# Performance work log

Measured on AMD Instinct MI355X. Metric: run time of the kernel, lower is better.

## Reference

```python
import jax, jax.numpy as jnp
import numpy as np

PADDING = 2  # matches init_kwargs; kernel_size = 2*PADDING + 1 -> no circular wrap in roll trick


def setup_inputs() -> dict:
    key = jax.random.key(0)
    k1, k2, k3 = jax.random.split(key, 3)
    x = jax.random.normal(k1, (16, 512, 4096), dtype=jnp.float32)
    weight = jax.random.normal(k2, (512, 512, 5), dtype=jnp.float32)
    bias = jax.random.normal(k3, (512,), dtype=jnp.float32)
    return {"x": x, "weight": weight, "bias": bias}


def reference(x, weight, bias):
    # Original torch module: pad(p,p) -> cat of roll(n-p) copies -> slice -> matmul.
    # Index algebra: out[b,o,t] = sum_{c,n} w[o,c,n] * xpad[b,c, t + 2p - n],
    # which (with kernel_size == 2p+1, so no circular wraparound) is a true
    # convolution, i.e. cross-correlation with the kernel flipped along taps.
    w_flipped = jnp.flip(weight, axis=-1)  # [O, I, K]
    y = jax.lax.conv_general_dilated(
        x, w_flipped,
        window_strides=(1,),
        padding=[(PADDING, PADDING)],
        dimension_numbers=("NCH", "OIH", "NCH"),
    )  # [B, O, T]
    return y + bias[None, :, None]
```

## Files before the change

### kernel.cpp

```cpp
#include <hip/hip_runtime.h>
#include <hip/hip_bf16.h>

typedef __attribute__((ext_vector_type(8))) short short8;
typedef __attribute__((ext_vector_type(4))) float f32x4;

#define B_   16
#define O_   512
#define C_   512
#define T_   4096
#define TP   (T_ + 32)
#define KT   5
#define BM   128
#define BN   512
#define BK   32
#define NCHUNK (C_/BK)
#define AFR  40
#define BGR  33

__device__ __forceinline__ void gload_lds16(const void* g, void* l) {
    __builtin_amdgcn_global_load_lds(
        (const __attribute__((address_space(1))) unsigned int*)g,
        (__attribute__((address_space(3))) unsigned int*)l, 16, 0, 0);
}

__global__ void wrepack_kernel(const float* __restrict__ w, unsigned short* __restrict__ wb) {
    int e = blockIdx.x * 256 + threadIdx.x;
    if (e >= KT * O_ * C_) return;
    int n   = e / (O_ * C_);
    int rem = e % (O_ * C_);
    int o   = rem / C_;
    int c   = rem % C_;
    float v = w[((size_t)o * C_ + c) * KT + n];
    __hip_bfloat16 h = __float2bfloat16(v);
    wb[e] = *reinterpret_cast<unsigned short*>(&h);
}

__global__ void padzero_kernel(unsigned short* __restrict__ xt) {
    int i = blockIdx.x * 256 + threadIdx.x;
    if (i >= B_ * 32 * C_) return;
    int b = i / (32 * C_);
    int r = (i / C_) % 32;
    int c = i % C_;
    int tp = (r < 16) ? r : (T_ + r);
    xt[((size_t)b * TP + tp) * C_ + c] = 0;
}

__global__ void xtrans_kernel(const float* __restrict__ x, unsigned short* __restrict__ xt) {
    __shared__ float tile[64][65];
    int b  = blockIdx.z;
    int c0 = blockIdx.y * 64;
    int t0 = blockIdx.x * 64;
    const float* xb = x + ((size_t)b * C_ + c0) * T_ + t0;
#pragma unroll
    for (int p = 0; p < 4; ++p) {
        int idx = p * 256 + threadIdx.x;
        int cl = idx >> 4;
        int tj = (idx & 15) << 2;
        float4 v = *reinterpret_cast<const float4*>(xb + (size_t)cl * T_ + tj);
        tile[cl][tj + 0] = v.x;
        tile[cl][tj + 1] = v.y;
        tile[cl][tj + 2] = v.z;
        tile[cl][tj + 3] = v.w;
    }
    __syncthreads();
    unsigned short* xtb = xt + ((size_t)b * TP + 16 + t0) * C_ + c0;
#pragma unroll
    for (int p = 0; p < 2; ++p) {
        int g  = p * 256 + threadIdx.x;
        int tl = g >> 3;
        int cj = (g & 7) << 3;
        unsigned short tmp[8];
#pragma unroll
        for (int i = 0; i < 8; ++i) {
            __hip_bfloat16 h = __float2bfloat16(tile[cj + i][tl]);
            tmp[i] = *reinterpret_cast<unsigned short*>(&h);
        }
        *reinterpret_cast<short8*>(xtb + (size_t)tl * C_ + cj) =
            *reinterpret_cast<const short8*>(tmp);
    }
}

__global__ __launch_bounds__(512, 2) void conv_gemm_kernel(
        const unsigned short* __restrict__ wb,
        const unsigned short* __restrict__ xt,
        const float* __restrict__ bias,
        float* __restrict__ out) {
    __shared__ unsigned short a_lds[2][AFR * 512];
    __shared__ unsigned short b_lds[2][BGR * 512];

    int bid = blockIdx.x;
    int swz = (bid & 7) * 64 + (bid >> 3);
    int o0  = (swz & 3) * BM;
    int t0  = ((swz >> 2) & 7) * BN;
    int b   = swz >> 5;

    int tid  = threadIdx.x;
    int lane = tid & 63;
    int wid  = tid >> 6;
    int lr   = lane & 15;
    int lg   = lane >> 4;

    int bo[KT][4];
#pragma unroll
    for (int n = 0; n < KT; ++n)
#pragma unroll
        for (int ni = 0; ni < 4; ++ni) {
            int row = wid * 64 + ni * 16 + lr + 4 - n;
            bo[n][ni] = row * 32 + ((lg ^ ((row >> 1) & 3)) << 3);
        }

    f32x4 acc[8][4];
#pragma unroll
    for (int mi = 0; mi < 8; ++mi)
#pragma unroll
        for (int ni = 0; ni < 4; ++ni)
            acc[mi][ni] = (f32x4)0.0f;

    const unsigned short* ag = wb + (size_t)(o0 + lr) * C_ + lg * 8;
    int c8 = (lane & 3) ^ ((lane >> 3) & 3);
    const unsigned short* bg = xt + ((size_t)b * TP + (t0 + 14 + (lane >> 2))) * C_ + c8 * 8;

#pragma unroll
    for (int f = wid; f < AFR; f += 8)
        gload_lds16(ag + (size_t)((f >> 3) * O_ + (f & 7) * 16) * C_, &a_lds[0][f * 512]);
#pragma unroll
    for (int j = wid; j < BGR; j += 8)
        gload_lds16(bg + (size_t)(j * 16) * C_, &b_lds[0][j * 512]);
    asm volatile("s_waitcnt vmcnt(0)" ::: "memory");
    __builtin_amdgcn_s_barrier();

    for (int chunk = 0; chunk < NCHUNK; ++chunk) {
        int cur = chunk & 1;
        int c1  = (chunk + 1) * BK;
        bool pf = (chunk + 1 < NCHUNK);

#pragma unroll
        for (int n = 0; n < KT; ++n) {
            short8 af[8], bf[4];
#pragma unroll
            for (int mi = 0; mi < 8; ++mi)
                af[mi] = *reinterpret_cast<const short8*>(
                    &a_lds[cur][(n * 8 + mi) * 512 + lane * 8]);
#pragma unroll
            for (int ni = 0; ni < 4; ++ni)
                bf[ni] = *reinterpret_cast<const short8*>(&b_lds[cur][bo[n][ni]]);

            if (pf) {
                int f = n * 8 + wid;
                gload_lds16(ag + (size_t)((f >> 3) * O_ + (f & 7) * 16) * C_ + c1,
                            &a_lds[cur ^ 1][f * 512]);
                int j = n * 8 + wid;
                if (j < BGR)
                    gload_lds16(bg + (size_t)(j * 16) * C_ + c1, &b_lds[cur ^ 1][j * 512]);
            }

            __builtin_amdgcn_s_barrier();
            asm volatile("s_waitcnt lgkmcnt(0)" ::: "memory");
            __builtin_amdgcn_sched_barrier(0);

            __builtin_amdgcn_s_setprio(1);
#pragma unroll
            for (int mi = 0; mi < 8; ++mi)
#pragma unroll
                for (int ni = 0; ni < 4; ++ni)
                    acc[mi][ni] = __builtin_amdgcn_mfma_f32_16x16x32_bf16(
                        af[mi], bf[ni], acc[mi][ni], 0, 0, 0);
            __builtin_amdgcn_s_setprio(0);
        }

        asm volatile("s_waitcnt vmcnt(0)" ::: "memory");
        __builtin_amdgcn_s_barrier();
    }

#pragma unroll
    for (int mi = 0; mi < 8; ++mi) {
#pragma unroll
        for (int ni = 0; ni < 4; ++ni) {
            int orow = o0 + mi * 16 + lg * 4;
            int tcol = t0 + wid * 64 + ni * 16 + lr;
#pragma unroll
            for (int r = 0; r < 4; ++r) {
                out[((size_t)b * O_ + orow + r) * T_ + tcol] =
                    acc[mi][ni][r] + bias[orow + r];
            }
        }
    }
}

extern "C" void kernel_launch(void* const* d_in, const int* in_sizes, int n_in,
                              void* d_out, int out_size, void* d_ws, size_t ws_size,
                              hipStream_t stream) {
    const float* x    = (const float*)d_in[0];
    const float* w    = (const float*)d_in[1];
    const float* bias = (const float*)d_in[2];
    float* out        = (float*)d_out;

    unsigned short* wb  = (unsigned short*)d_ws;
    unsigned short* xtp = wb + (size_t)KT * O_ * C_;

    padzero_kernel<<<(B_ * 32 * C_ + 255) / 256, 256, 0, stream>>>(xtp);
    wrepack_kernel<<<(KT * O_ * C_ + 255) / 256, 256, 0, stream>>>(w, wb);
    xtrans_kernel<<<dim3(T_ / 64, C_ / 64, B_), 256, 0, stream>>>(x, xtp);
    conv_gemm_kernel<<<512, 512, 0, stream>>>(wb, xtp, bias, out);
}
```

Baseline: 193.6 us.

## Issue all chunk prefetches up front and double-buffer tap fragments in registers

All global-to-LDS prefetches for the next chunk are now issued at the start of each chunk instead of being spread across the five taps. The per-tap barrier and lgkmcnt wait are removed. LDS fragment loads are ping-ponged between two register sets so the next tap's reads overlap the current tap's MFMAs. This cuts four barriers per chunk and adds software pipelining, at the cost of more VGPR pressure from holding two fragment sets alongside the 128-float accumulator under launch_bounds(512,2).

After: 199.6 us. +3.1%, slower.

```diff
diff --git a/kernel.cpp b/kernel.cpp
--- a/kernel.cpp
+++ b/kernel.cpp
@@ -80,6 +80,29 @@
     }
 }
 
+#define LOADTAP(n, AF, BF)                                                         \
+    do {                                                                           \
+        _Pragma("unroll")                                                          \
+        for (int mi = 0; mi < 8; ++mi)                                             \
+            AF[mi] = *reinterpret_cast<const short8*>(                             \
+                &al[((n) * 8 + mi) * 512 + lane * 8]);                             \
+        _Pragma("unroll")                                                          \
+        for (int ni = 0; ni < 4; ++ni)                                             \
+            BF[ni] = *reinterpret_cast<const short8*>(&bl[bo[(n)][ni]]);           \
+    } while (0)
+
+#define MFMATAP(AF, BF)                                                            \
+    do {                                                                           \
+        __builtin_amdgcn_s_setprio(1);                                             \
+        _Pragma("unroll")                                                          \
+        for (int mi = 0; mi < 8; ++mi)                                             \
+            _Pragma("unroll")                                                      \
+            for (int ni = 0; ni < 4; ++ni)                                         \
+                acc[mi][ni] = __builtin_amdgcn_mfma_f32_16x16x32_bf16(             \
+                    AF[mi], BF[ni], acc[mi][ni], 0, 0, 0);                         \
+        __builtin_amdgcn_s_setprio(0);                                             \
+    } while (0)
+
 __global__ __launch_bounds__(512, 2) void conv_gemm_kernel(
         const unsigned short* __restrict__ wb,
         const unsigned short* __restrict__ xt,
@@ -121,55 +144,50 @@
     const unsigned short* bg = xt + ((size_t)b * TP + (t0 + 14 + (lane >> 2))) * C_ + c8 * 8;
 
 #pragma unroll
-    for (int f = wid; f < AFR; f += 8)
-        gload_lds16(ag + (size_t)((f >> 3) * O_ + (f & 7) * 16) * C_, &a_lds[0][f * 512]);
-#pragma unroll
-    for (int j = wid; j < BGR; j += 8)
-        gload_lds16(bg + (size_t)(j * 16) * C_, &b_lds[0][j * 512]);
+    for (int k = 0; k < 5; ++k)
+        gload_lds16(ag + (size_t)(k * O_ + wid * 16) * C_, &a_lds[0][(wid + 8 * k) * 512]);
+#pragma unroll
+    for (int k = 0; k < 5; ++k) {
+        int j = wid + 8 * k;
+        if (j < BGR)
+            gload_lds16(bg + (size_t)(j * 16) * C_, &b_lds[0][j * 512]);
+    }
     asm volatile("s_waitcnt vmcnt(0)" ::: "memory");
     __builtin_amdgcn_s_barrier();
 
     for (int chunk = 0; chunk < NCHUNK; ++chunk) {
         int cur = chunk & 1;
-        int c1  = (chunk + 1) * BK;
-        bool pf = (chunk + 1 < NCHUNK);
-
-#pragma unroll
-        for (int n = 0; n < KT; ++n) {
-            short8 af[8], bf[4];
-#pragma unroll
-            for (int mi = 0; mi < 8; ++mi)
-                af[mi] = *reinterpret_cast<const short8*>(
-                    &a_lds[cur][(n * 8 + mi) * 512 + lane * 8]);
-#pragma unroll
-            for (int ni = 0; ni < 4; ++ni)
-                bf[ni] = *reinterpret_cast<const short8*>(&b_lds[cur][bo[n][ni]]);
-
-            if (pf) {
-                int f = n * 8 + wid;
-                gload_lds16(ag + (size_t)((f >> 3) * O_ + (f & 7) * 16) * C_ + c1,
-                            &a_lds[cur ^ 1][f * 512]);
-                int j = n * 8 + wid;
+        const unsigned short* al = a_lds[cur];
+        const unsigned short* bl = b_lds[cur];
+
+        if (chunk + 1 < NCHUNK) {
+            int c1 = (chunk + 1) * BK;
+#pragma unroll
+            for (int k = 0; k < 5; ++k)
+                gload_lds16(ag + (size_t)(k * O_ + wid * 16) * C_ + c1,
+                            &a_lds[cur ^ 1][(wid + 8 * k) * 512]);
+#pragma unroll
+            for (int k = 0; k < 5; ++k) {
+                int j = wid + 8 * k;
                 if (j < BGR)
                     gload_lds16(bg + (size_t)(j * 16) * C_ + c1, &b_lds[cur ^ 1][j * 512]);
             }
-
-            __builtin_amdgcn_s_barrier();
-            asm volatile("s_waitcnt lgkmcnt(0)" ::: "memory");
-            __builtin_amdgcn_sched_barrier(0);
-
-            __builtin_amdgcn_s_setprio(1);
-#pragma unroll
-            for (int mi = 0; mi < 8; ++mi)
-#pragma unroll
-                for (int ni = 0; ni < 4; ++ni)
-                    acc[mi][ni] = __builtin_amdgcn_mfma_f32_16x16x32_bf16(
-                        af[mi], bf[ni], acc[mi][ni], 0, 0, 0);
-            __builtin_amdgcn_s_setprio(0);
-        }
+        }
+
+        short8 af0[8], bf0[4], af1[8], bf1[4];
+        LOADTAP(0, af0, bf0);
+        LOADTAP(1, af1, bf1);
+        MFMATAP(af0, bf0);
+        LOADTAP(2, af0, bf0);
+        MFMATAP(af1, bf1);
+        LOADTAP(3, af1, bf1);
+        MFMATAP(af0, bf0);
+        LOADTAP(4, af0, bf0);
+        MFMATAP(af1, bf1);
+        MFMATAP(af0, bf0);
 
         asm volatile("s_waitcnt vmcnt(0)" ::: "memory");
-        __builtin_amdgcn_s_barrier();
+        __syncthreads();
     }
 
 #pragma unroll
```

## Switch conv GEMM to 32x32x16 MFMA tiles and fuse prep kernels

Applied to the files above, without the earlier changes.

The main GEMM moves from 16x16x32 bf16 MFMA to 32x32x16 MFMA. That change reworks the LDS fragment layout, the B-row swizzle and the global-to-LDS load mapping, and uses 4x2 accumulators of 16 floats each. The larger MFMA shape is meant to cut the LDS fragment reads per FLOP and the instruction-issue overhead. The weight repack and pad-zero kernels are also merged into one launch to save a kernel launch. The risks are a changed LDS bank-conflict pattern from the new swizzle and a less coalesced output store pattern in the epilogue.

Result: slower. 202.9 us (+4.8%).

```diff
diff --git a/kernel.cpp b/kernel.cpp
--- a/kernel.cpp
+++ b/kernel.cpp
@@ -2,7 +2,7 @@
 #include <hip/hip_bf16.h>
 
 typedef __attribute__((ext_vector_type(8))) short short8;
-typedef __attribute__((ext_vector_type(4))) float f32x4;
+typedef __attribute__((ext_vector_type(16))) float f32x16;
 
 #define B_   16
 #define O_   512
@@ -14,7 +14,6 @@
 #define BN   512
 #define BK   32
 #define NCHUNK (C_/BK)
-#define AFR  40
 #define BGR  33
 
 __device__ __forceinline__ void gload_lds16(const void* g, void* l) {
@@ -23,26 +22,27 @@
         (__attribute__((address_space(3))) unsigned int*)l, 16, 0, 0);
 }
 
-__global__ void wrepack_kernel(const float* __restrict__ w, unsigned short* __restrict__ wb) {
-    int e = blockIdx.x * 256 + threadIdx.x;
-    if (e >= KT * O_ * C_) return;
-    int n   = e / (O_ * C_);
-    int rem = e % (O_ * C_);
-    int o   = rem / C_;
-    int c   = rem % C_;
-    float v = w[((size_t)o * C_ + c) * KT + n];
-    __hip_bfloat16 h = __float2bfloat16(v);
-    wb[e] = *reinterpret_cast<unsigned short*>(&h);
-}
-
-__global__ void padzero_kernel(unsigned short* __restrict__ xt) {
-    int i = blockIdx.x * 256 + threadIdx.x;
-    if (i >= B_ * 32 * C_) return;
-    int b = i / (32 * C_);
-    int r = (i / C_) % 32;
-    int c = i % C_;
-    int tp = (r < 16) ? r : (T_ + r);
-    xt[((size_t)b * TP + tp) * C_ + c] = 0;
+__global__ void prep_kernel(const float* __restrict__ w,
+                            unsigned short* __restrict__ wb,
+                            unsigned short* __restrict__ xt) {
+    int bid = blockIdx.x;
+    if (bid < 5120) {
+        int e   = bid * 256 + threadIdx.x;
+        int n   = e / (O_ * C_);
+        int rem = e % (O_ * C_);
+        int o   = rem / C_;
+        int c   = rem % C_;
+        float v = w[((size_t)o * C_ + c) * KT + n];
+        __hip_bfloat16 h = __float2bfloat16(v);
+        wb[e] = *reinterpret_cast<unsigned short*>(&h);
+    } else {
+        int i = (bid - 5120) * 256 + threadIdx.x;
+        int b = i / (32 * C_);
+        int r = (i / C_) % 32;
+        int c = i % C_;
+        int tp = (r < 16) ? r : (T_ + r);
+        xt[((size_t)b * TP + tp) * C_ + c] = 0;
+    }
 }
 
 __global__ void xtrans_kernel(const float* __restrict__ x, unsigned short* __restrict__ xt) {
@@ -85,70 +85,85 @@
         const unsigned short* __restrict__ xt,
         const float* __restrict__ bias,
         float* __restrict__ out) {
-    __shared__ unsigned short a_lds[2][AFR * 512];
+    __shared__ unsigned short a_lds[2][40 * 512];
     __shared__ unsigned short b_lds[2][BGR * 512];
 
-    int bid = blockIdx.x;
-    int swz = (bid & 7) * 64 + (bid >> 3);
-    int o0  = (swz & 3) * BM;
-    int t0  = ((swz >> 2) & 7) * BN;
-    int b   = swz >> 5;
+    int bid  = blockIdx.x;
+    int swzb = (bid & 7) * 64 + (bid >> 3);
+    int o0   = (swzb & 3) * BM;
+    int t0   = ((swzb >> 2) & 7) * BN;
+    int b    = swzb >> 5;
 
     int tid  = threadIdx.x;
     int lane = tid & 63;
     int wid  = tid >> 6;
-    int lr   = lane & 15;
-    int lg   = lane >> 4;
-
-    int bo[KT][4];
+    int l31  = lane & 31;
+    int lh   = lane >> 5;
+
+    int bo[KT][2][2];
 #pragma unroll
     for (int n = 0; n < KT; ++n)
 #pragma unroll
-        for (int ni = 0; ni < 4; ++ni) {
-            int row = wid * 64 + ni * 16 + lr + 4 - n;
-            bo[n][ni] = row * 32 + ((lg ^ ((row >> 1) & 3)) << 3);
-        }
-
-    f32x4 acc[8][4];
-#pragma unroll
-    for (int mi = 0; mi < 8; ++mi)
-#pragma unroll
-        for (int ni = 0; ni < 4; ++ni)
-            acc[mi][ni] = (f32x4)0.0f;
-
-    const unsigned short* ag = wb + (size_t)(o0 + lr) * C_ + lg * 8;
-    int c8 = (lane & 3) ^ ((lane >> 3) & 3);
+        for (int ni = 0; ni < 2; ++ni)
+#pragma unroll
+            for (int ks = 0; ks < 2; ++ks) {
+                int row = wid * 64 + ni * 32 + l31 + 4 - n;
+                int sw  = ((row >> 1) ^ (row >> 3)) & 3;
+                bo[n][ni][ks] = row * 32 + ((((ks << 1) + lh) ^ sw) << 3);
+            }
+
+    f32x16 acc[4][2];
+#pragma unroll
+    for (int mi = 0; mi < 4; ++mi)
+#pragma unroll
+        for (int ni = 0; ni < 2; ++ni)
+            acc[mi][ni] = (f32x16)0.0f;
+
+    const unsigned short* ag = wb + (size_t)(o0 + l31) * C_ + lh * 8;
+    int c8 = (lane & 3) ^ ((lane >> 3) & 3) ^ ((2 * (wid & 1) + lh) & 3);
     const unsigned short* bg = xt + ((size_t)b * TP + (t0 + 14 + (lane >> 2))) * C_ + c8 * 8;
 
-#pragma unroll
-    for (int f = wid; f < AFR; f += 8)
-        gload_lds16(ag + (size_t)((f >> 3) * O_ + (f & 7) * 16) * C_, &a_lds[0][f * 512]);
-#pragma unroll
-    for (int j = wid; j < BGR; j += 8)
-        gload_lds16(bg + (size_t)(j * 16) * C_, &b_lds[0][j * 512]);
+    int wmi = wid >> 1;
+    int wks = wid & 1;
+
+#pragma unroll
+    for (int k = 0; k < KT; ++k)
+        gload_lds16(ag + (size_t)(k * O_ + wmi * 32) * C_ + wks * 16,
+                    &a_lds[0][(k * 8 + wid) * 512]);
+#pragma unroll
+    for (int k = 0; k < 5; ++k) {
+        int j = wid + 8 * k;
+        if (j < BGR)
+            gload_lds16(bg + (size_t)(j * 16) * C_, &b_lds[0][j * 512]);
+    }
     asm volatile("s_waitcnt vmcnt(0)" ::: "memory");
     __builtin_amdgcn_s_barrier();
 
     for (int chunk = 0; chunk < NCHUNK; ++chunk) {
         int cur = chunk & 1;
-        int c1  = (chunk + 1) * BK;
+        const unsigned short* al = a_lds[cur];
+        const unsigned short* bl = b_lds[cur];
+        int  c1 = (chunk + 1) * BK;
         bool pf = (chunk + 1 < NCHUNK);
 
 #pragma unroll
         for (int n = 0; n < KT; ++n) {
-            short8 af[8], bf[4];
-#pragma unroll
-            for (int mi = 0; mi < 8; ++mi)
-                af[mi] = *reinterpret_cast<const short8*>(
-                    &a_lds[cur][(n * 8 + mi) * 512 + lane * 8]);
-#pragma unroll
-            for (int ni = 0; ni < 4; ++ni)
-                bf[ni] = *reinterpret_cast<const short8*>(&b_lds[cur][bo[n][ni]]);
+            short8 af[4][2], bf[2][2];
+#pragma unroll
+            for (int mi = 0; mi < 4; ++mi)
+#pragma unroll
+                for (int ks = 0; ks < 2; ++ks)
+                    af[mi][ks] = *reinterpret_cast<const short8*>(
+                        &al[(n * 8 + mi * 2 + ks) * 512 + lane * 8]);
+#pragma unroll
+            for (int ni = 0; ni < 2; ++ni)
+#pragma unroll
+                for (int ks = 0; ks < 2; ++ks)
+                    bf[ni][ks] = *reinterpret_cast<const short8*>(&bl[bo[n][ni][ks]]);
 
             if (pf) {
-                int f = n * 8 + wid;
-                gload_lds16(ag + (size_t)((f >> 3) * O_ + (f & 7) * 16) * C_ + c1,
-                            &a_lds[cur ^ 1][f * 512]);
+                gload_lds16(ag + (size_t)(n * O_ + wmi * 32) * C_ + wks * 16 + c1,
+                            &a_lds[cur ^ 1][(n * 8 + wid) * 512]);
                 int j = n * 8 + wid;
                 if (j < BGR)
                     gload_lds16(bg + (size_t)(j * 16) * C_ + c1, &b_lds[cur ^ 1][j * 512]);
@@ -160,11 +175,13 @@
 
             __builtin_amdgcn_s_setprio(1);
 #pragma unroll
-            for (int mi = 0; mi < 8; ++mi)
-#pragma unroll
-                for (int ni = 0; ni < 4; ++ni)
-                    acc[mi][ni] = __builtin_amdgcn_mfma_f32_16x16x32_bf16(
-                        af[mi], bf[ni], acc[mi][ni], 0, 0, 0);
+            for (int mi = 0; mi < 4; ++mi)
+#pragma unroll
+                for (int ni = 0; ni < 2; ++ni)
+#pragma unroll
+                    for (int ks = 0; ks < 2; ++ks)
+                        acc[mi][ni] = __builtin_amdgcn_mfma_f32_32x32x16_bf16(
+                            af[mi][ks], bf[ni][ks], acc[mi][ni], 0, 0, 0);
             __builtin_amdgcn_s_setprio(0);
         }
 
@@ -173,15 +190,15 @@
     }
 
 #pragma unroll
-    for (int mi = 0; mi < 8; ++mi) {
-#pragma unroll
-        for (int ni = 0; ni < 4; ++ni) {
-            int orow = o0 + mi * 16 + lg * 4;
-            int tcol = t0 + wid * 64 + ni * 16 + lr;
-#pragma unroll
-            for (int r = 0; r < 4; ++r) {
-                out[((size_t)b * O_ + orow + r) * T_ + tcol] =
-                    acc[mi][ni][r] + bias[orow + r];
+    for (int mi = 0; mi < 4; ++mi) {
+#pragma unroll
+        for (int ni = 0; ni < 2; ++ni) {
+            int tcol = t0 + wid * 64 + ni * 32 + l31;
+#pragma unroll
+            for (int r = 0; r < 16; ++r) {
+                int orow = o0 + mi * 32 + (r & 3) + 8 * (r >> 2) + 4 * lh;
+                out[((size_t)b * O_ + orow) * T_ + tcol] =
+                    acc[mi][ni][r] + bias[orow];
             }
         }
     }
@@ -198,8 +215,7 @@
     unsigned short* wb  = (unsigned short*)d_ws;
     unsigned short* xtp = wb + (size_t)KT * O_ * C_;
 
-    padzero_kernel<<<(B_ * 32 * C_ + 255) / 256, 256, 0, stream>>>(xtp);
-    wrepack_kernel<<<(KT * O_ * C_ + 255) / 256, 256, 0, stream>>>(w, wb);
+    prep_kernel<<<6144, 256, 0, stream>>>(w, wb, xtp);
     xtrans_kernel<<<dim3(T_ / 64, C_ / 64, B_), 256, 0, stream>>>(x, xtp);
     conv_gemm_kernel<<<512, 512, 0, stream>>>(wb, xtp, bias, out);
 }
```

## Shrink GEMM tile to 64x256 with 4 waves and fuse prep kernels

Applied to the files above, without the earlier changes.

The conv GEMM tile shrinks from 128x512 (8 waves) to 64x256 (4 waves), giving 2048 blocks instead of 512, and the per-tap prefetch schedule is redistributed across taps 0-2. The padding-zero and weight-repack kernels are merged into one launch. The smaller tile aims to improve occupancy and load balance across CUs, but it lowers operand reuse per block and so raises LDS and global traffic per FLOP.

Result: slower. 204.4 us (+5.6%).

```diff
diff --git a/kernel.cpp b/kernel.cpp
--- a/kernel.cpp
+++ b/kernel.cpp
@@ -10,12 +10,12 @@
 #define T_   4096
 #define TP   (T_ + 32)
 #define KT   5
-#define BM   128
-#define BN   512
+#define BM   64
+#define BN   256
 #define BK   32
 #define NCHUNK (C_/BK)
-#define AFR  40
-#define BGR  33
+#define AFRG 20
+#define BGRP 17
 
 __device__ __forceinline__ void gload_lds16(const void* g, void* l) {
     __builtin_amdgcn_global_load_lds(
@@ -23,26 +23,27 @@
         (__attribute__((address_space(3))) unsigned int*)l, 16, 0, 0);
 }
 
-__global__ void wrepack_kernel(const float* __restrict__ w, unsigned short* __restrict__ wb) {
-    int e = blockIdx.x * 256 + threadIdx.x;
-    if (e >= KT * O_ * C_) return;
-    int n   = e / (O_ * C_);
-    int rem = e % (O_ * C_);
-    int o   = rem / C_;
-    int c   = rem % C_;
-    float v = w[((size_t)o * C_ + c) * KT + n];
-    __hip_bfloat16 h = __float2bfloat16(v);
-    wb[e] = *reinterpret_cast<unsigned short*>(&h);
-}
-
-__global__ void padzero_kernel(unsigned short* __restrict__ xt) {
-    int i = blockIdx.x * 256 + threadIdx.x;
-    if (i >= B_ * 32 * C_) return;
-    int b = i / (32 * C_);
-    int r = (i / C_) % 32;
-    int c = i % C_;
-    int tp = (r < 16) ? r : (T_ + r);
-    xt[((size_t)b * TP + tp) * C_ + c] = 0;
+__global__ void prep_kernel(const float* __restrict__ w,
+                            unsigned short* __restrict__ wb,
+                            unsigned short* __restrict__ xt) {
+    int bid = blockIdx.x;
+    if (bid < 5120) {
+        int e   = bid * 256 + threadIdx.x;
+        int n   = e / (O_ * C_);
+        int rem = e % (O_ * C_);
+        int o   = rem / C_;
+        int c   = rem % C_;
+        float v = w[((size_t)o * C_ + c) * KT + n];
+        __hip_bfloat16 h = __float2bfloat16(v);
+        wb[e] = *reinterpret_cast<unsigned short*>(&h);
+    } else {
+        int i = (bid - 5120) * 256 + threadIdx.x;
+        int b = i / (32 * C_);
+        int r = (i / C_) % 32;
+        int c = i % C_;
+        int tp = (r < 16) ? r : (T_ + r);
+        xt[((size_t)b * TP + tp) * C_ + c] = 0;
+    }
 }
 
 __global__ void xtrans_kernel(const float* __restrict__ x, unsigned short* __restrict__ xt) {
@@ -80,19 +81,19 @@
     }
 }
 
-__global__ __launch_bounds__(512, 2) void conv_gemm_kernel(
+__global__ __launch_bounds__(256, 2) void conv_gemm_kernel(
         const unsigned short* __restrict__ wb,
         const unsigned short* __restrict__ xt,
         const float* __restrict__ bias,
         float* __restrict__ out) {
-    __shared__ unsigned short a_lds[2][AFR * 512];
-    __shared__ unsigned short b_lds[2][BGR * 512];
-
-    int bid = blockIdx.x;
-    int swz = (bid & 7) * 64 + (bid >> 3);
-    int o0  = (swz & 3) * BM;
-    int t0  = ((swz >> 2) & 7) * BN;
-    int b   = swz >> 5;
+    __shared__ unsigned short a_lds[2][AFRG * 512];
+    __shared__ unsigned short b_lds[2][BGRP * 512];
+
+    int bid  = blockIdx.x;
+    int swz  = (bid & 7) * 256 + (bid >> 3);
+    int o0   = (swz & 7) * BM;
+    int t0   = ((swz >> 3) & 15) * BN;
+    int b    = swz >> 7;
 
     int tid  = threadIdx.x;
     int lane = tid & 63;
@@ -109,9 +110,9 @@
             bo[n][ni] = row * 32 + ((lg ^ ((row >> 1) & 3)) << 3);
         }
 
-    f32x4 acc[8][4];
-#pragma unroll
-    for (int mi = 0; mi < 8; ++mi)
+    f32x4 acc[4][4];
+#pragma unroll
+    for (int mi = 0; mi < 4; ++mi)
 #pragma unroll
         for (int ni = 0; ni < 4; ++ni)
             acc[mi][ni] = (f32x4)0.0f;
@@ -121,37 +122,58 @@
     const unsigned short* bg = xt + ((size_t)b * TP + (t0 + 14 + (lane >> 2))) * C_ + c8 * 8;
 
 #pragma unroll
-    for (int f = wid; f < AFR; f += 8)
-        gload_lds16(ag + (size_t)((f >> 3) * O_ + (f & 7) * 16) * C_, &a_lds[0][f * 512]);
-#pragma unroll
-    for (int j = wid; j < BGR; j += 8)
-        gload_lds16(bg + (size_t)(j * 16) * C_, &b_lds[0][j * 512]);
+    for (int k = 0; k < 5; ++k) {
+        int f = wid + 4 * k;
+        gload_lds16(ag + (size_t)((f >> 2) * O_ + (f & 3) * 16) * C_, &a_lds[0][f * 512]);
+    }
+#pragma unroll
+    for (int k = 0; k < 5; ++k) {
+        int j = wid + 4 * k;
+        if (j < BGRP)
+            gload_lds16(bg + (size_t)(j * 16) * C_, &b_lds[0][j * 512]);
+    }
     asm volatile("s_waitcnt vmcnt(0)" ::: "memory");
     __builtin_amdgcn_s_barrier();
 
     for (int chunk = 0; chunk < NCHUNK; ++chunk) {
         int cur = chunk & 1;
-        int c1  = (chunk + 1) * BK;
+        const unsigned short* al = a_lds[cur];
+        const unsigned short* bl = b_lds[cur];
+        int  c1 = (chunk + 1) * BK;
         bool pf = (chunk + 1 < NCHUNK);
 
 #pragma unroll
         for (int n = 0; n < KT; ++n) {
-            short8 af[8], bf[4];
-#pragma unroll
-            for (int mi = 0; mi < 8; ++mi)
+            short8 af[4], bf[4];
+#pragma unroll
+            for (int mi = 0; mi < 4; ++mi)
                 af[mi] = *reinterpret_cast<const short8*>(
-                    &a_lds[cur][(n * 8 + mi) * 512 + lane * 8]);
+                    &al[(n * 4 + mi) * 512 + lane * 8]);
 #pragma unroll
             for (int ni = 0; ni < 4; ++ni)
-                bf[ni] = *reinterpret_cast<const short8*>(&b_lds[cur][bo[n][ni]]);
+                bf[ni] = *reinterpret_cast<const short8*>(&bl[bo[n][ni]]);
 
             if (pf) {
-                int f = n * 8 + wid;
-                gload_lds16(ag + (size_t)((f >> 3) * O_ + (f & 7) * 16) * C_ + c1,
-                            &a_lds[cur ^ 1][f * 512]);
-                int j = n * 8 + wid;
-                if (j < BGR)
+                if (n == 0) {
+#pragma unroll
+                    for (int k = 0; k < 5; ++k) {
+                        int f = wid + 4 * k;
+                        gload_lds16(ag + (size_t)((f >> 2) * O_ + (f & 3) * 16) * C_ + c1,
+                                    &a_lds[cur ^ 1][f * 512]);
+                    }
+                } else if (n == 1) {
+#pragma unroll
+                    for (int k = 0; k < 3; ++k) {
+                        int j = wid + 4 * k;
+                        gload_lds16(bg + (size_t)(j * 16) * C_ + c1, &b_lds[cur ^ 1][j * 512]);
+                    }
+                } else if (n == 2) {
+                    int j = 12 + wid;
                     gload_lds16(bg + (size_t)(j * 16) * C_ + c1, &b_lds[cur ^ 1][j * 512]);
+                    if (wid == 0)
+                        gload_lds16(bg + (size_t)(16 * 16) * C_ + c1,
+                                    &b_lds[cur ^ 1][16 * 512]);
+                }
             }
 
             __builtin_amdgcn_s_barrier();
@@ -160,7 +182,7 @@
 
             __builtin_amdgcn_s_setprio(1);
 #pragma unroll
-            for (int mi = 0; mi < 8; ++mi)
+            for (int mi = 0; mi < 4; ++mi)
 #pragma unroll
                 for (int ni = 0; ni < 4; ++ni)
                     acc[mi][ni] = __builtin_amdgcn_mfma_f32_16x16x32_bf16(
@@ -173,7 +195,7 @@
     }
 
 #pragma unroll
-    for (int mi = 0; mi < 8; ++mi) {
+    for (int mi = 0; mi < 4; ++mi) {
 #pragma unroll
         for (int ni = 0; ni < 4; ++ni) {
             int orow = o0 + mi * 16 + lg * 4;
@@ -198,8 +220,7 @@
     unsigned short* wb  = (unsigned short*)d_ws;
     unsigned short* xtp = wb + (size_t)KT * O_ * C_;
 
-    padzero_kernel<<<(B_ * 32 * C_ + 255) / 256, 256, 0, stream>>>(xtp);
-    wrepack_kernel<<<(KT * O_ * C_ + 255) / 256, 256, 0, stream>>>(w, wb);
+    prep_kernel<<<6144, 256, 0, stream>>>(w, wb, xtp);
     xtrans_kernel<<<dim3(T_ / 64, C_ / 64, B_), 256, 0, stream>>>(x, xtp);
-    conv_gemm_kernel<<<512, 512, 0, stream>>>(wb, xtp, bias, out);
-}
+    conv_gemm_kernel<<<2048, 256, 0, stream>>>(wb, xtp, bias, out);
+}
```
